# Performance work log

Measured on AMD Instinct MI355X. Metric: run time of the kernel, lower is better.

## Reference

```python
import jax, jax.numpy as jnp
import numpy as np

B, T, DFEAT = 2, 2048, 1024
DIM, DEPTH, H, DH = 512, 2, 8, 64
INNER = H * DH  # 512
MLP = 512
RED1, RED2 = DIM // 16, DIM // 32  # 32, 16
EPS = 1e-5


def _ln(x, g, b):
    m = jnp.mean(x, axis=-1, keepdims=True)
    v = jnp.mean((x - m) ** 2, axis=-1, keepdims=True)
    return (x - m) * jax.lax.rsqrt(v + EPS) * g + b


def _bn_eval(x, g, b, rm, rv):
    # x: [B, C, T]; eval-mode BatchNorm1d with running stats
    return (x - rm[:, None]) * jax.lax.rsqrt(rv[:, None] + EPS) * g[:, None] + b[:, None]


def setup_inputs() -> dict:
    key = jax.random.key(0)
    ks = iter(jax.random.split(key, 64))
    rn = lambda shape, s=0.02: (jax.random.normal(next(ks), shape, dtype=jnp.float32) * s)
    inp = {}
    inp['x'] = jax.random.normal(next(ks), (B, T, DFEAT), dtype=jnp.float32)
    # Temporal embedding conv (k=3, pad=1), OIW layout
    inp['emb_w'] = rn((DIM, DFEAT, 3))
    inp['emb_b'] = jnp.zeros((DIM,), jnp.float32)
    # Transformer: stacked per-layer params [DEPTH, ...]
    inp['ln1_g'] = jnp.ones((DEPTH, DIM), jnp.float32)
    inp['ln1_b'] = jnp.zeros((DEPTH, DIM), jnp.float32)
    inp['wqkvt'] = rn((DEPTH, DIM, 4 * INNER))
    inp['wout'] = rn((DEPTH, 2 * INNER, DIM))
    inp['bout'] = jnp.zeros((DEPTH, DIM), jnp.float32)
    inp['ln2_g'] = jnp.ones((DEPTH, DIM), jnp.float32)
    inp['ln2_b'] = jnp.zeros((DEPTH, DIM), jnp.float32)
    inp['w1'] = rn((DEPTH, DIM, MLP))
    inp['b1'] = jnp.zeros((DEPTH, MLP), jnp.float32)
    inp['w2'] = rn((DEPTH, MLP, DIM))
    inp['b2'] = jnp.zeros((DEPTH, DIM), jnp.float32)
    # NormalHead (k=1 convs -> pointwise), eval-mode BN params
    inp['h1_w'] = rn((RED1, DIM)); inp['h1_b'] = jnp.zeros((RED1,), jnp.float32)
    inp['bn1_g'] = jnp.ones((RED1,), jnp.float32); inp['bn1_b'] = jnp.zeros((RED1,), jnp.float32)
    inp['bn1_m'] = jnp.zeros((RED1,), jnp.float32); inp['bn1_v'] = jnp.ones((RED1,), jnp.float32)
    inp['h2_w'] = rn((RED2, RED1)); inp['h2_b'] = jnp.zeros((RED2,), jnp.float32)
    inp['bn2_g'] = jnp.ones((RED2,), jnp.float32); inp['bn2_b'] = jnp.zeros((RED2,), jnp.float32)
    inp['bn2_m'] = jnp.zeros((RED2,), jnp.float32); inp['bn2_v'] = jnp.ones((RED2,), jnp.float32)
    inp['h3_w'] = rn((1, RED2)); inp['h3_b'] = jnp.zeros((1,), jnp.float32)
    return inp


def _attention(x, wqkvt, wout, bout, attn2):
    b, n, d = x.shape
    qkvt = x @ wqkvt  # [b, n, 4*INNER]
    q, k, v, t = jnp.split(qkvt, 4, axis=-1)
    sp = lambda z: z.reshape(b, n, H, DH).transpose(0, 2, 1, 3)  # b h n d
    q, k, v, t = sp(q), sp(k), sp(v), sp(t)
    scale = DH ** -0.5
    dots = jnp.einsum('bhid,bhjd->bhij', q, k) * scale
    attn1 = jax.nn.softmax(dots, axis=-1)
    out1 = jnp.einsum('bhij,bhjd->bhid', attn1, v)
    out2 = jnp.einsum('ij,bhjd->bhid', attn2, t)
    out = jnp.concatenate([out1, out2], axis=-1)  # b h n 2*DH
    out = out.transpose(0, 2, 1, 3).reshape(b, n, 2 * INNER)
    return out @ wout + bout


def _forward(x, emb_w, emb_b, ln1_g, ln1_b, wqkvt, wout, bout, ln2_g, ln2_b,
             w1, b1, w2, b2, h1_w, h1_b, bn1_g, bn1_b, bn1_m, bn1_v,
             h2_w, h2_b, bn2_g, bn2_b, bn2_m, bn2_v, h3_w, h3_b):
    # Temporal embedding: Conv1d(k=3,pad=1) + ReLU over time axis
    xc = x.transpose(0, 2, 1)  # [B, DFEAT, T]
    emb = jax.lax.conv_general_dilated(xc, emb_w, (1,), 'SAME',
                                       dimension_numbers=('NCH', 'OIH', 'NCH'))
    emb = jax.nn.relu(emb + emb_b[None, :, None])
    h = emb.transpose(0, 2, 1)  # [B, T, DIM]
    # fixed temporal-decay attention matrix (batch/head independent)
    idx = jnp.arange(T, dtype=jnp.float32)
    tg = jnp.abs(idx[None, :] - idx[:, None])
    a2 = jnp.exp(-tg / jnp.float32(np.e))
    attn2 = a2 / a2.sum(-1)  # torch broadcast: divide along last axis
    for l in range(DEPTH):
        h = h + _attention(_ln(h, ln1_g[l], ln1_b[l]), wqkvt[l], wout[l], bout[l], attn2)
        z = _ln(h, ln2_g[l], ln2_b[l])
        z = jax.nn.gelu(z @ w1[l] + b1[l], approximate=False) @ w2[l] + b2[l]
        h = h + z
    # NormalHead on [B, DIM, T] with k=1 convs
    y = h.transpose(0, 2, 1)
    f1 = jnp.einsum('oc,bct->bot', h1_w, y) + h1_b[None, :, None]
    f2 = jnp.einsum('oc,bct->bot', h2_w, jax.nn.relu(_bn_eval(f1, bn1_g, bn1_b, bn1_m, bn1_v))) + h2_b[None, :, None]
    f3 = jnp.einsum('oc,bct->bot', h3_w, jax.nn.relu(_bn_eval(f2, bn2_g, bn2_b, bn2_m, bn2_v))) + h3_b[None, :, None]
    scores = jax.nn.sigmoid(f3)[:, 0, :]  # [B, T]
    return scores


def reference(x, emb_w, emb_b, ln1_g, ln1_b, wqkvt, wout, bout, ln2_g, ln2_b,
              w1, b1, w2, b2, h1_w, h1_b, bn1_g, bn1_b, bn1_m, bn1_v,
              h2_w, h2_b, bn2_g, bn2_b, bn2_m, bn2_v, h3_w, h3_b):
    return _forward(x, emb_w, emb_b, ln1_g, ln1_b, wqkvt, wout, bout, ln2_g, ln2_b,
                    w1, b1, w2, b2, h1_w, h1_b, bn1_g, bn1_b, bn1_m, bn1_v,
                    h2_w, h2_b, bn2_g, bn2_b, bn2_m, bn2_v, h3_w, h3_b)
```

## Files before the change

### kernel.cpp

```cpp
#include <hip/hip_runtime.h>
#include <hip/hip_bf16.h>
#include <math.h>

#define TN 2048
#define BN 2
#define DF 1024
#define DM 512
#define NHD 8
#define DHD 64
#define INV_E 0.36787944117144233f
#define R_DECAY 0.69220062755534635f

typedef float f32x4 __attribute__((ext_vector_type(4)));
typedef __bf16 bf16x8 __attribute__((ext_vector_type(8)));
typedef unsigned short ushort8 __attribute__((ext_vector_type(8)));
typedef unsigned short ushort4v __attribute__((ext_vector_type(4)));
typedef unsigned int u32x4 __attribute__((ext_vector_type(4)));
typedef unsigned short u16;
typedef unsigned int u32;

__device__ inline u16 f2bf(float f) {
    __hip_bfloat16 b = __float2bfloat16(f);
    return __builtin_bit_cast(u16, b);
}
__device__ inline float bf2f(u16 u) {
    unsigned int x = ((unsigned int)u) << 16;
    return __builtin_bit_cast(float, x);
}
__device__ inline bf16x8 ldbf8(const u16* p) {
    return __builtin_bit_cast(bf16x8, *(const ushort8*)p);
}

struct WtrAll {
    const float* src[8];
    u16* dst[8];
    int K[8], N[8], start[8], mask[8], shift[8];
};

__global__ __launch_bounds__(256) void wtr_all_kernel(WtrAll a) {
    __shared__ u16 tile[64][67];
    int bid = blockIdx.x;
    int w = 0;
#pragma unroll
    for (int i = 1; i < 8; ++i)
        if (bid >= a.start[i]) w = i;
    const float* src = a.src[w];
    u16* dst = a.dst[w];
    int K = a.K[w], N = a.N[w];
    int t0 = bid - a.start[w];
    int bx = t0 & a.mask[w], by = t0 >> a.shift[w];
    int t = threadIdx.x;
    int tr = t >> 4, tc = (t & 15) * 4;
#pragma unroll
    for (int rr = 0; rr < 4; ++rr) {
        int kl = tr + rr * 16;
        float4 v = *(const float4*)&src[(size_t)(by * 64 + kl) * N + bx * 64 + tc];
        tile[kl][tc + 0] = f2bf(v.x);
        tile[kl][tc + 1] = f2bf(v.y);
        tile[kl][tc + 2] = f2bf(v.z);
        tile[kl][tc + 3] = f2bf(v.w);
    }
    __syncthreads();
#pragma unroll
    for (int rr = 0; rr < 4; ++rr) {
        int nl = tr + rr * 16;
        ushort4v o;
#pragma unroll
        for (int q = 0; q < 4; ++q) o[q] = tile[tc + q][nl];
        *(ushort4v*)&dst[(size_t)(bx * 64 + nl) * K + by * 64 + tc] = o;
    }
}

__global__ __launch_bounds__(256) void emb_tr_kernel(const float* __restrict__ w,
                                                     u16* __restrict__ dst) {
    int idx = blockIdx.x * 256 + threadIdx.x;
    if (idx >= DM * 3 * DF) return;
    int o = idx / (3 * DF);
    int rem = idx - o * 3 * DF;
    int tap = rem / DF, i = rem - tap * DF;
    dst[idx] = f2bf(w[(size_t)o * 3 * DF + i * 3 + tap]);
}

__global__ __launch_bounds__(256) void sinv_kernel(float* __restrict__ sinv) {
    int j = blockIdx.x * 256 + threadIdx.x;
    if (j >= TN) return;
    float r = __expf(-INV_E);
    float inv1mr = 1.f / (1.f - r);
    float a = (1.f - __expf(-(float)(j + 1) * INV_E)) * inv1mr;
    float b = (r - __expf(-(float)(TN - j) * INV_E)) * inv1mr;
    sinv[j] = 1.f / (a + b);
}

__global__ __launch_bounds__(256) void xshift_kernel(const float* __restrict__ x,
                                                     u16* __restrict__ xs) {
    int idx = blockIdx.x * 256 + threadIdx.x;
    if (idx >= BN * TN * 3 * DF / 8) return;
    int row = idx / (3 * DF / 8);
    int kc = (idx - row * (3 * DF / 8)) * 8;
    int b = row >> 11, t = row & (TN - 1);
    int tap = kc / DF, i = kc - tap * DF;
    int tt = t + tap - 1;
    ushort8 o;
    if (tt < 0 || tt >= TN) {
        for (int q = 0; q < 8; ++q) o[q] = 0;
    } else {
        const float4* p = (const float4*)&x[((size_t)b * TN + tt) * DF + i];
        float4 v0 = p[0], v1 = p[1];
        o[0] = f2bf(v0.x); o[1] = f2bf(v0.y); o[2] = f2bf(v0.z); o[3] = f2bf(v0.w);
        o[4] = f2bf(v1.x); o[5] = f2bf(v1.y); o[6] = f2bf(v1.z); o[7] = f2bf(v1.w);
    }
    *(ushort8*)&xs[(size_t)row * 3 * DF + kc] = o;
}

template <int MODE, int BM, int BNT>
__global__ __launch_bounds__(256) void gemm2(const u16* __restrict__ A,
                                             const u16* __restrict__ Bt,
                                             const float* __restrict__ bias,
                                             const float* resid, void* outp,
                                             int M, int N, int K) {
    constexpr int MR = BM / 32, NR = BNT / 32;
    constexpr int PA = BM / 64, PB = BNT / 64;
    __shared__ __align__(16) u16 As[2][BM][72];
    __shared__ __align__(16) u16 Bs[2][BNT][72];
    int tid = threadIdx.x;
    int lane = tid & 63, wid = tid >> 6;
    int m0 = blockIdx.y * BM, n0 = blockIdx.x * BNT;
    int wm = (wid >> 1) * (BM / 2), wn = (wid & 1) * (BNT / 2);
    int fr = lane & 15, kq = (lane >> 4) * 8;
    int srow = tid >> 2, scol = (tid & 3) * 16;
    f32x4 acc[MR][NR] = {};
    const u16* Ap = A + (size_t)(m0 + srow) * K + scol;
    const u16* Bp = Bt + (size_t)(n0 + srow) * K + scol;
    ushort8 ra[PA][2], rb[PB][2];
#pragma unroll
    for (int p = 0; p < PA; ++p) {
        ra[p][0] = *(const ushort8*)(Ap + (size_t)p * 64 * K);
        ra[p][1] = *(const ushort8*)(Ap + (size_t)p * 64 * K + 8);
    }
#pragma unroll
    for (int p = 0; p < PB; ++p) {
        rb[p][0] = *(const ushort8*)(Bp + (size_t)p * 64 * K);
        rb[p][1] = *(const ushort8*)(Bp + (size_t)p * 64 * K + 8);
    }
    int nt = K >> 6;
    int pb = 0;
    for (int t = 0; t < nt; ++t) {
#pragma unroll
        for (int p = 0; p < PA; ++p) {
            *(ushort8*)&As[pb][srow + p * 64][scol] = ra[p][0];
            *(ushort8*)&As[pb][srow + p * 64][scol + 8] = ra[p][1];
        }
#pragma unroll
        for (int p = 0; p < PB; ++p) {
            *(ushort8*)&Bs[pb][srow + p * 64][scol] = rb[p][0];
            *(ushort8*)&Bs[pb][srow + p * 64][scol + 8] = rb[p][1];
        }
        __syncthreads();
        if (t + 1 < nt) {
            int ko = (t + 1) << 6;
#pragma unroll
            for (int p = 0; p < PA; ++p) {
                ra[p][0] = *(const ushort8*)(Ap + (size_t)p * 64 * K + ko);
                ra[p][1] = *(const ushort8*)(Ap + (size_t)p * 64 * K + ko + 8);
            }
#pragma unroll
            for (int p = 0; p < PB; ++p) {
                rb[p][0] = *(const ushort8*)(Bp + (size_t)p * 64 * K + ko);
                rb[p][1] = *(const ushort8*)(Bp + (size_t)p * 64 * K + ko + 8);
            }
        }
#pragma unroll
        for (int kc = 0; kc < 2; ++kc) {
            bf16x8 af[MR], bf[NR];
#pragma unroll
            for (int a = 0; a < MR; ++a) af[a] = ldbf8(&As[pb][wm + a * 16 + fr][kc * 32 + kq]);
#pragma unroll
            for (int b = 0; b < NR; ++b) bf[b] = ldbf8(&Bs[pb][wn + b * 16 + fr][kc * 32 + kq]);
#pragma unroll
            for (int a = 0; a < MR; ++a)
#pragma unroll
                for (int b = 0; b < NR; ++b)
                    acc[a][b] = __builtin_amdgcn_mfma_f32_16x16x32_bf16(af[a], bf[b], acc[a][b], 0, 0, 0);
        }
        pb ^= 1;
    }
    int rq = (lane >> 4) * 4;
#pragma unroll
    for (int a = 0; a < MR; ++a)
#pragma unroll
        for (int b = 0; b < NR; ++b) {
            int col = n0 + wn + b * 16 + fr;
            float bv = (MODE & 1) ? bias[col] : 0.f;
#pragma unroll
            for (int r = 0; r < 4; ++r) {
                int row = m0 + wm + a * 16 + rq + r;
                float v = acc[a][b][r] + bv;
                if (MODE & 2) v = fmaxf(v, 0.f);
                if (MODE & 4) v = 0.5f * v * (1.f + erff(v * 0.7071067811865476f));
                if (MODE & 8) v += resid[(size_t)row * N + col];
                if (MODE & 16) ((float*)outp)[(size_t)row * N + col] = v;
                else           ((u16*)outp)[(size_t)row * N + col] = f2bf(v);
            }
        }
}

__global__ __launch_bounds__(256) void ln_kernel(const float* __restrict__ h,
                                                 const float* __restrict__ g,
                                                 const float* __restrict__ bta,
                                                 u16* __restrict__ outp) {
    int lane = threadIdx.x & 63, wid = threadIdx.x >> 6;
    int row = blockIdx.x * 4 + wid;
    const float4* xp = (const float4*)(h + (size_t)row * DM + lane * 8);
    float4 v0 = xp[0], v1 = xp[1];
    float v[8] = {v0.x, v0.y, v0.z, v0.w, v1.x, v1.y, v1.z, v1.w};
    float s = 0.f;
#pragma unroll
    for (int i = 0; i < 8; ++i) s += v[i];
    for (int sft = 1; sft < 64; sft <<= 1) s += __shfl_xor(s, sft, 64);
    float mean = s * (1.f / DM);
    float q = 0.f;
#pragma unroll
    for (int i = 0; i < 8; ++i) { float d = v[i] - mean; q += d * d; }
    for (int sft = 1; sft < 64; sft <<= 1) q += __shfl_xor(q, sft, 64);
    float rs = rsqrtf(q * (1.f / DM) + 1e-5f);
    ushort8 o;
#pragma unroll
    for (int i = 0; i < 8; ++i) {
        float y = (v[i] - mean) * rs * g[lane * 8 + i] + bta[lane * 8 + i];
        o[i] = f2bf(y);
    }
    *(ushort8*)&outp[(size_t)row * DM + lane * 8] = o;
}

__global__ __launch_bounds__(256, 6) void attn_split(const u16* __restrict__ qkvt,
                                                     u16* __restrict__ po,
                                                     float* __restrict__ pl) {
    __shared__ __align__(16) u16 Ks[64][72];
    __shared__ __align__(16) u16 Vs[64][72];
    int tid = threadIdx.x;
    int lane = tid & 63, wid = tid >> 6;
    int bid = blockIdx.x;
    int cc = bid & 3, qb = (bid >> 2) & 31, hh = (bid >> 7) & 7, b = bid >> 10;
    int fr = lane & 15, kq = (lane >> 4) * 8, rq = (lane >> 4) * 4;

    int qrow = qb * 64 + wid * 16 + fr;
    bf16x8 aq[2];
#pragma unroll
    for (int kc = 0; kc < 2; ++kc) {
        bf16x8 t = ldbf8(&qkvt[((size_t)(b * TN + qrow)) * 2048 + hh * 64 + kc * 32 + kq]);
        bf16x8 sc;
#pragma unroll
        for (int i = 0; i < 8; ++i) sc[i] = (__bf16)(0.125f * (float)t[i]);
        aq[kc] = sc;
    }

    f32x4 o[4];
#pragma unroll
    for (int cb = 0; cb < 4; ++cb) o[cb] = f32x4{0.f, 0.f, 0.f, 0.f};
    float rsum = 0.f;

    int srow = tid >> 3, scol = (tid & 7) * 8;
    int vxw = ((scol >> 3) & 7) << 3;
    int i01 = (fr + ((lane & 16) << 1)) << 2;
    int i23 = i01 + 64;
    bool hi2 = (lane & 32) != 0;

    const u16* kvbase = qkvt + ((size_t)(b * TN + cc * 512 + srow)) * 2048 + hh * 64 + scol;

    ushort8 rk[2], rv[2];
    rk[0] = *(const ushort8*)(kvbase + 512);
    rk[1] = *(const ushort8*)(kvbase + 512 + (size_t)32 * 2048);
    rv[0] = *(const ushort8*)(kvbase + 1024);
    rv[1] = *(const ushort8*)(kvbase + 1024 + (size_t)32 * 2048);

    for (int t = 0; t < 8; ++t) {
        __syncthreads();
#pragma unroll
        for (int half = 0; half < 2; ++half) {
            int jr = srow + half * 32;
            *(ushort8*)&Ks[jr][scol] = rk[half];
            int jc = jr ^ vxw;
#pragma unroll
            for (int i = 0; i < 8; ++i) Vs[scol + i][jc] = rv[half][i];
        }
        __syncthreads();
        if (t < 7) {
            const u16* kb2 = kvbase + (size_t)(t + 1) * 64 * 2048;
            rk[0] = *(const ushort8*)(kb2 + 512);
            rk[1] = *(const ushort8*)(kb2 + 512 + (size_t)32 * 2048);
            rv[0] = *(const ushort8*)(kb2 + 1024);
            rv[1] = *(const ushort8*)(kb2 + 1024 + (size_t)32 * 2048);
        }
        u32 pkr[4][2];
#pragma unroll
        for (int jb = 0; jb < 4; ++jb) {
            f32x4 sa = f32x4{0.f, 0.f, 0.f, 0.f};
#pragma unroll
            for (int kc = 0; kc < 2; ++kc) {
                bf16x8 bk = ldbf8(&Ks[jb * 16 + fr][kc * 32 + kq]);
                sa = __builtin_amdgcn_mfma_f32_16x16x32_bf16(bk, aq[kc], sa, 0, 0, 0);
            }
            float p0 = __expf(sa[0]), p1 = __expf(sa[1]);
            float p2 = __expf(sa[2]), p3 = __expf(sa[3]);
            rsum += (p0 + p1) + (p2 + p3);
            pkr[jb][0] = ((u32)f2bf(p1) << 16) | (u32)f2bf(p0);
            pkr[jb][1] = ((u32)f2bf(p3) << 16) | (u32)f2bf(p2);
        }
        bf16x8 pa[2];
#pragma unroll
        for (int kc = 0; kc < 2; ++kc) {
            u32 a0 = (u32)__builtin_amdgcn_ds_bpermute(i01, (int)pkr[kc * 2][0]);
            u32 b0 = (u32)__builtin_amdgcn_ds_bpermute(i01, (int)pkr[kc * 2 + 1][0]);
            u32 a1 = (u32)__builtin_amdgcn_ds_bpermute(i01, (int)pkr[kc * 2][1]);
            u32 b1 = (u32)__builtin_amdgcn_ds_bpermute(i01, (int)pkr[kc * 2 + 1][1]);
            u32 a2 = (u32)__builtin_amdgcn_ds_bpermute(i23, (int)pkr[kc * 2][0]);
            u32 b2 = (u32)__builtin_amdgcn_ds_bpermute(i23, (int)pkr[kc * 2 + 1][0]);
            u32 a3 = (u32)__builtin_amdgcn_ds_bpermute(i23, (int)pkr[kc * 2][1]);
            u32 b3 = (u32)__builtin_amdgcn_ds_bpermute(i23, (int)pkr[kc * 2 + 1][1]);
            u32x4 w;
            w[0] = hi2 ? b0 : a0;
            w[1] = hi2 ? b1 : a1;
            w[2] = hi2 ? b2 : a2;
            w[3] = hi2 ? b3 : a3;
            pa[kc] = __builtin_bit_cast(bf16x8, w);
        }
#pragma unroll
        for (int cb = 0; cb < 4; ++cb)
#pragma unroll
            for (int kc = 0; kc < 2; ++kc) {
                int vrow = cb * 16 + fr;
                bf16x8 bv = ldbf8(&Vs[vrow][(kc * 32 + kq) ^ (((vrow >> 3) & 7) << 3)]);
                o[cb] = __builtin_amdgcn_mfma_f32_16x16x32_bf16(pa[kc], bv, o[cb], 0, 0, 0);
            }
    }
    rsum += __shfl_xor(rsum, 16, 64);
    rsum += __shfl_xor(rsum, 32, 64);
#pragma unroll
    for (int r = 0; r < 4; ++r) {
        int grow = (b * NHD + hh) * TN + qb * 64 + wid * 16 + rq + r;
        size_t pidx = (size_t)grow * 4 + cc;
#pragma unroll
        for (int cb = 0; cb < 4; ++cb)
            po[pidx * 64 + cb * 16 + fr] = f2bf(o[cb][r]);
    }
    if (lane < 16) {
        int grow = (b * NHD + hh) * TN + qb * 64 + wid * 16 + fr;
        pl[(size_t)grow * 4 + cc] = rsum;
    }
}

#define BCH 32
__global__ __launch_bounds__(256) void postattn_kernel(const u16* __restrict__ po,
                                                       const float* __restrict__ pl,
                                                       const u16* __restrict__ qkvt,
                                                       const float* __restrict__ sinv,
                                                       u16* __restrict__ attcat) {
    int bid = blockIdx.x;
    if (bid < BN * NHD * TN / 4) {
        int lane = threadIdx.x & 63, wid = threadIdx.x >> 6;
        int R = bid * 4 + wid;
        float l = 0.f, ov = 0.f;
#pragma unroll
        for (int cc = 0; cc < 4; ++cc) {
            l += pl[R * 4 + cc];
            ov += bf2f(po[((size_t)R * 4 + cc) * 64 + lane]);
        }
        int bh = R >> 11, q = R & (TN - 1);
        int b = bh >> 3, hh = bh & 7;
        attcat[((size_t)(b * TN + q)) * 1024 + hh * 128 + lane] = f2bf(ov / l);
    } else {
        int t2 = (bid - BN * NHD * TN / 4) * 256 + threadIdx.x;
        int c = t2 & 511;
        int rest = t2 >> 9;
        int chunk = rest & 63;
        int b = rest >> 6;
        int i0 = chunk * BCH;
        const float r = R_DECAY;
        const u16* tcol = qkvt + 1536 + c;
        float regs[BCH];
        float st = 0.f;
        for (int j = i0 - 32; j < i0; ++j) {
            if (j >= 0) st = r * st + sinv[j] * bf2f(tcol[(size_t)(b * TN + j) * 2048]);
        }
#pragma unroll
        for (int k = 0; k < BCH; ++k) {
            int j = i0 + k;
            st = r * st + sinv[j] * bf2f(tcol[(size_t)(b * TN + j) * 2048]);
            regs[k] = st;
        }
        st = 0.f;
        for (int j = i0 + BCH + 31; j >= i0 + BCH; --j) {
            if (j < TN) st = r * st + sinv[j] * bf2f(tcol[(size_t)(b * TN + j) * 2048]);
        }
#pragma unroll
        for (int k = BCH - 1; k >= 0; --k) {
            int j = i0 + k;
            regs[k] += r * st;
            st = r * st + sinv[j] * bf2f(tcol[(size_t)(b * TN + j) * 2048]);
        }
        int outcol = (c >> 6) * 128 + 64 + (c & 63);
#pragma unroll
        for (int k = 0; k < BCH; ++k)
            attcat[((size_t)(b * TN + i0 + k)) * 1024 + outcol] = f2bf(regs[k]);
    }
}

__global__ __launch_bounds__(256) void head_kernel(
    const float* __restrict__ h, const float* __restrict__ h1w, const float* __restrict__ h1b,
    const float* __restrict__ bn1g, const float* __restrict__ bn1b,
    const float* __restrict__ bn1m, const float* __restrict__ bn1v,
    const float* __restrict__ h2w, const float* __restrict__ h2b,
    const float* __restrict__ bn2g, const float* __restrict__ bn2b,
    const float* __restrict__ bn2m, const float* __restrict__ bn2v,
    const float* __restrict__ h3w, const float* __restrict__ h3b,
    float* __restrict__ outp) {
    int lane = threadIdx.x & 63, wid = threadIdx.x >> 6;
    int idx = blockIdx.x * 4 + wid;
    const float4* xp = (const float4*)(h + (size_t)idx * DM + lane * 8);
    float4 v0 = xp[0], v1 = xp[1];
    float v[8] = {v0.x, v0.y, v0.z, v0.w, v1.x, v1.y, v1.z, v1.w};
    float a1[32];
#pragma unroll
    for (int o = 0; o < 32; ++o) {
        const float4* wp = (const float4*)(h1w + (size_t)o * DM + lane * 8);
        float4 w0 = wp[0], w1v = wp[1];
        a1[o] = w0.x * v[0] + w0.y * v[1] + w0.z * v[2] + w0.w * v[3] +
                w1v.x * v[4] + w1v.y * v[5] + w1v.z * v[6] + w1v.w * v[7];
    }
    for (int sft = 1; sft < 64; sft <<= 1) {
#pragma unroll
        for (int o = 0; o < 32; ++o) a1[o] += __shfl_xor(a1[o], sft, 64);
    }
    float r1[32];
#pragma unroll
    for (int o = 0; o < 32; ++o) {
        float f = a1[o] + h1b[o];
        f = (f - bn1m[o]) * rsqrtf(bn1v[o] + 1e-5f) * bn1g[o] + bn1b[o];
        r1[o] = fmaxf(f, 0.f);
    }
    float r2[16];
#pragma unroll
    for (int p = 0; p < 16; ++p) {
        float s = h2b[p];
#pragma unroll
        for (int o = 0; o < 32; ++o) s = fmaf(h2w[p * 32 + o], r1[o], s);
        s = (s - bn2m[p]) * rsqrtf(bn2v[p] + 1e-5f) * bn2g[p] + bn2b[p];
        r2[p] = fmaxf(s, 0.f);
    }
    float f3 = h3b[0];
#pragma unroll
    for (int p = 0; p < 16; ++p) f3 = fmaf(h3w[p], r2[p], f3);
    if (lane == 0) outp[idx] = 1.f / (1.f + __expf(-f3));
}

extern "C" void kernel_launch(void* const* d_in, const int* in_sizes, int n_in,
                              void* d_out, int out_size, void* d_ws, size_t ws_size,
                              hipStream_t stream) {
    const float* x     = (const float*)d_in[0];
    const float* emb_w = (const float*)d_in[1];
    const float* emb_b = (const float*)d_in[2];
    const float* ln1_g = (const float*)d_in[3];
    const float* ln1_b = (const float*)d_in[4];
    const float* wqkvt = (const float*)d_in[5];
    const float* wout  = (const float*)d_in[6];
    const float* bout  = (const float*)d_in[7];
    const float* ln2_g = (const float*)d_in[8];
    const float* ln2_b = (const float*)d_in[9];
    const float* w1    = (const float*)d_in[10];
    const float* b1    = (const float*)d_in[11];
    const float* w2    = (const float*)d_in[12];
    const float* b2    = (const float*)d_in[13];
    const float* h1w   = (const float*)d_in[14];
    const float* h1b   = (const float*)d_in[15];
    const float* bn1g  = (const float*)d_in[16];
    const float* bn1b  = (const float*)d_in[17];
    const float* bn1m  = (const float*)d_in[18];
    const float* bn1v  = (const float*)d_in[19];
    const float* h2w   = (const float*)d_in[20];
    const float* h2b   = (const float*)d_in[21];
    const float* bn2g  = (const float*)d_in[22];
    const float* bn2b  = (const float*)d_in[23];
    const float* bn2m  = (const float*)d_in[24];
    const float* bn2v  = (const float*)d_in[25];
    const float* h3w   = (const float*)d_in[26];
    const float* h3b   = (const float*)d_in[27];
    float* outp = (float*)d_out;

    char* ws = (char*)d_ws;
    size_t off = 0;
    auto take = [&](size_t bytes) {
        char* p = ws + off;
        off = (off + bytes + 255) & ~(size_t)255;
        return p;
    };
    const size_t MB = 1024 * 1024;
    float* h    = (float*)take((size_t)BN * TN * DM * 4);
    char* Pr    = take(18 * MB);
    u16* attcat = (u16*)take((size_t)BN * TN * 1024 * 2);
    float* sinv = (float*)take(TN * 4);
    u16* embwt  = (u16*)take((size_t)DM * 3 * DF * 2);
    u16* wqt    = (u16*)take((size_t)2 * 2048 * DM * 2);
    u16* woutt  = (u16*)take((size_t)2 * DM * 1024 * 2);
    u16* w1t    = (u16*)take((size_t)2 * DM * DM * 2);
    u16* w2t    = (u16*)take((size_t)2 * DM * DM * 2);
    u16* U      = (u16*)take((size_t)BN * TN * 3 * DF * 2);
    u16* xs = U;
    u16* qkvtb = U;
    u16* xln  = (u16*)Pr;
    u16* z1   = (u16*)(Pr + 4 * MB);
    float* pl = (float*)Pr;
    u16* po   = (u16*)(Pr + 1 * MB);
    (void)ws_size; (void)in_sizes; (void)n_in; (void)out_size;

    emb_tr_kernel<<<dim3(DM * 3 * DF / 256), dim3(256), 0, stream>>>(emb_w, embwt);
    {
        WtrAll a;
        int cur = 0;
        for (int l = 0; l < 2; ++l) {
            int e = l * 4;
            a.src[e + 0] = wqkvt + (size_t)l * 512 * 2048; a.dst[e + 0] = wqt + (size_t)l * 2048 * 512;
            a.K[e + 0] = 512;  a.N[e + 0] = 2048; a.start[e + 0] = cur; a.mask[e + 0] = 31; a.shift[e + 0] = 5; cur += 256;
            a.src[e + 1] = wout + (size_t)l * 1024 * 512;  a.dst[e + 1] = woutt + (size_t)l * 512 * 1024;
            a.K[e + 1] = 1024; a.N[e + 1] = 512;  a.start[e + 1] = cur; a.mask[e + 1] = 7;  a.shift[e + 1] = 3; cur += 128;
            a.src[e + 2] = w1 + (size_t)l * 512 * 512;     a.dst[e + 2] = w1t + (size_t)l * 512 * 512;
            a.K[e + 2] = 512;  a.N[e + 2] = 512;  a.start[e + 2] = cur; a.mask[e + 2] = 7;  a.shift[e + 2] = 3; cur += 64;
            a.src[e + 3] = w2 + (size_t)l * 512 * 512;     a.dst[e + 3] = w2t + (size_t)l * 512 * 512;
            a.K[e + 3] = 512;  a.N[e + 3] = 512;  a.start[e + 3] = cur; a.mask[e + 3] = 7;  a.shift[e + 3] = 3; cur += 64;
        }
        wtr_all_kernel<<<dim3(cur), dim3(256), 0, stream>>>(a);
    }
    sinv_kernel<<<dim3(TN / 256), dim3(256), 0, stream>>>(sinv);
    xshift_kernel<<<dim3(BN * TN * 3 * DF / 8 / 256), dim3(256), 0, stream>>>(x, xs);

    gemm2<19, 64, 64><<<dim3(DM / 64, BN * TN / 64), dim3(256), 0, stream>>>(
        xs, embwt, emb_b, nullptr, h, BN * TN, DM, 3 * DF);

    for (int l = 0; l < 2; ++l) {
        ln_kernel<<<dim3(BN * TN / 4), dim3(256), 0, stream>>>(h, ln1_g + l * DM, ln1_b + l * DM, xln);
        gemm2<0, 128, 128><<<dim3(2048 / 128, BN * TN / 128), dim3(256), 0, stream>>>(
            xln, wqt + (size_t)l * 2048 * 512, nullptr, nullptr, qkvtb, BN * TN, 2048, DM);
        attn_split<<<dim3(BN * NHD * (TN / 64) * 4), dim3(256), 0, stream>>>(qkvtb, po, pl);
        postattn_kernel<<<dim3(BN * NHD * TN / 4 + BN * 512 * (TN / BCH) / 256), dim3(256), 0, stream>>>(
            po, pl, qkvtb, sinv, attcat);
        gemm2<25, 64, 64><<<dim3(DM / 64, BN * TN / 64), dim3(256), 0, stream>>>(
            attcat, woutt + (size_t)l * 512 * 1024, bout + l * DM, h, h, BN * TN, DM, 1024);
        ln_kernel<<<dim3(BN * TN / 4), dim3(256), 0, stream>>>(h, ln2_g + l * DM, ln2_b + l * DM, xln);
        gemm2<5, 64, 64><<<dim3(DM / 64, BN * TN / 64), dim3(256), 0, stream>>>(
            xln, w1t + (size_t)l * 512 * 512, b1 + l * DM, nullptr, z1, BN * TN, DM, DM);
        gemm2<25, 64, 64><<<dim3(DM / 64, BN * TN / 64), dim3(256), 0, stream>>>(
            z1, w2t + (size_t)l * 512 * 512, b2 + l * DM, h, h, BN * TN, DM, DM);
    }
    head_kernel<<<dim3(BN * TN / 4), dim3(256), 0, stream>>>(
        h, h1w, h1b, bn1g, bn1b, bn1m, bn1v, h2w, h2b, bn2g, bn2b, bn2m, bn2v, h3w, h3b, outp);
}
```

Baseline: 347.9 us.

## Load GEMM tiles directly to LDS with XOR swizzle, enlarge M tiles

Replaces the register-staged, double-buffered GEMM tile loading with global_load_lds, which writes directly into shared memory. An XOR swizzle on the 16-byte chunks avoids bank conflicts without padding. Most 64x64 GEMM launches move to 128x64 tiles. The aim is lower register pressure and fewer LDS write instructions, but the single buffer exposes load latency with two barriers per k-step, and the larger tiles halve the block count.

```diff
diff --git a/kernel.cpp b/kernel.cpp
--- a/kernel.cpp
+++ b/kernel.cpp
@@ -29,6 +29,11 @@
 }
 __device__ inline bf16x8 ldbf8(const u16* p) {
     return __builtin_bit_cast(bf16x8, *(const ushort8*)p);
+}
+__device__ inline void gl_lds16(const u16* g, u16* l) {
+    __builtin_amdgcn_global_load_lds(
+        (const __attribute__((address_space(1))) unsigned int*)g,
+        (__attribute__((address_space(3))) unsigned int*)l, 16, 0, 0);
 }
 
 struct WtrAll {
@@ -113,76 +118,59 @@
 }
 
 template <int MODE, int BM, int BNT>
-__global__ __launch_bounds__(256) void gemm2(const u16* __restrict__ A,
+__global__ __launch_bounds__(256) void gemm3(const u16* __restrict__ A,
                                              const u16* __restrict__ Bt,
                                              const float* __restrict__ bias,
                                              const float* resid, void* outp,
                                              int M, int N, int K) {
     constexpr int MR = BM / 32, NR = BNT / 32;
-    constexpr int PA = BM / 64, PB = BNT / 64;
-    __shared__ __align__(16) u16 As[2][BM][72];
-    __shared__ __align__(16) u16 Bs[2][BNT][72];
+    __shared__ __align__(16) u16 As[BM][64];
+    __shared__ __align__(16) u16 Bs[BNT][64];
     int tid = threadIdx.x;
     int lane = tid & 63, wid = tid >> 6;
     int m0 = blockIdx.y * BM, n0 = blockIdx.x * BNT;
     int wm = (wid >> 1) * (BM / 2), wn = (wid & 1) * (BNT / 2);
-    int fr = lane & 15, kq = (lane >> 4) * 8;
-    int srow = tid >> 2, scol = (tid & 3) * 16;
+    int fr = lane & 15, g = lane >> 4;
+    int lrow8 = lane >> 3, slot = lane & 7;
     f32x4 acc[MR][NR] = {};
-    const u16* Ap = A + (size_t)(m0 + srow) * K + scol;
-    const u16* Bp = Bt + (size_t)(n0 + srow) * K + scol;
-    ushort8 ra[PA][2], rb[PB][2];
-#pragma unroll
-    for (int p = 0; p < PA; ++p) {
-        ra[p][0] = *(const ushort8*)(Ap + (size_t)p * 64 * K);
-        ra[p][1] = *(const ushort8*)(Ap + (size_t)p * 64 * K + 8);
-    }
-#pragma unroll
-    for (int p = 0; p < PB; ++p) {
-        rb[p][0] = *(const ushort8*)(Bp + (size_t)p * 64 * K);
-        rb[p][1] = *(const ushort8*)(Bp + (size_t)p * 64 * K + 8);
-    }
     int nt = K >> 6;
-    int pb = 0;
     for (int t = 0; t < nt; ++t) {
-#pragma unroll
-        for (int p = 0; p < PA; ++p) {
-            *(ushort8*)&As[pb][srow + p * 64][scol] = ra[p][0];
-            *(ushort8*)&As[pb][srow + p * 64][scol + 8] = ra[p][1];
-        }
-#pragma unroll
-        for (int p = 0; p < PB; ++p) {
-            *(ushort8*)&Bs[pb][srow + p * 64][scol] = rb[p][0];
-            *(ushort8*)&Bs[pb][srow + p * 64][scol + 8] = rb[p][1];
-        }
+        int k0 = t << 6;
         __syncthreads();
-        if (t + 1 < nt) {
-            int ko = (t + 1) << 6;
-#pragma unroll
-            for (int p = 0; p < PA; ++p) {
-                ra[p][0] = *(const ushort8*)(Ap + (size_t)p * 64 * K + ko);
-                ra[p][1] = *(const ushort8*)(Ap + (size_t)p * 64 * K + ko + 8);
-            }
-#pragma unroll
-            for (int p = 0; p < PB; ++p) {
-                rb[p][0] = *(const ushort8*)(Bp + (size_t)p * 64 * K + ko);
-                rb[p][1] = *(const ushort8*)(Bp + (size_t)p * 64 * K + ko + 8);
-            }
-        }
+#pragma unroll
+        for (int ii = 0; ii < BM / 32; ++ii) {
+            int R0 = wid * (BM / 4) + ii * 8;
+            int r = R0 + lrow8;
+            const u16* gsrc = A + (size_t)(m0 + r) * K + k0 + ((slot ^ (r & 7)) * 8);
+            gl_lds16(gsrc, &As[R0][0]);
+        }
+#pragma unroll
+        for (int ii = 0; ii < BNT / 32; ++ii) {
+            int R0 = wid * (BNT / 4) + ii * 8;
+            int r = R0 + lrow8;
+            const u16* gsrc = Bt + (size_t)(n0 + r) * K + k0 + ((slot ^ (r & 7)) * 8);
+            gl_lds16(gsrc, &Bs[R0][0]);
+        }
+        __syncthreads();
 #pragma unroll
         for (int kc = 0; kc < 2; ++kc) {
             bf16x8 af[MR], bf[NR];
 #pragma unroll
-            for (int a = 0; a < MR; ++a) af[a] = ldbf8(&As[pb][wm + a * 16 + fr][kc * 32 + kq]);
-#pragma unroll
-            for (int b = 0; b < NR; ++b) bf[b] = ldbf8(&Bs[pb][wn + b * 16 + fr][kc * 32 + kq]);
+            for (int a = 0; a < MR; ++a) {
+                int R = wm + a * 16 + fr;
+                af[a] = ldbf8(&As[R][((kc * 4 + g) ^ (fr & 7)) * 8]);
+            }
+#pragma unroll
+            for (int b = 0; b < NR; ++b) {
+                int R = wn + b * 16 + fr;
+                bf[b] = ldbf8(&Bs[R][((kc * 4 + g) ^ (fr & 7)) * 8]);
+            }
 #pragma unroll
             for (int a = 0; a < MR; ++a)
 #pragma unroll
                 for (int b = 0; b < NR; ++b)
                     acc[a][b] = __builtin_amdgcn_mfma_f32_16x16x32_bf16(af[a], bf[b], acc[a][b], 0, 0, 0);
         }
-        pb ^= 1;
     }
     int rq = (lane >> 4) * 4;
 #pragma unroll
@@ -532,22 +520,22 @@
     sinv_kernel<<<dim3(TN / 256), dim3(256), 0, stream>>>(sinv);
     xshift_kernel<<<dim3(BN * TN * 3 * DF / 8 / 256), dim3(256), 0, stream>>>(x, xs);
 
-    gemm2<19, 64, 64><<<dim3(DM / 64, BN * TN / 64), dim3(256), 0, stream>>>(
+    gemm3<19, 128, 64><<<dim3(DM / 64, BN * TN / 128), dim3(256), 0, stream>>>(
         xs, embwt, emb_b, nullptr, h, BN * TN, DM, 3 * DF);
 
     for (int l = 0; l < 2; ++l) {
         ln_kernel<<<dim3(BN * TN / 4), dim3(256), 0, stream>>>(h, ln1_g + l * DM, ln1_b + l * DM, xln);
-        gemm2<0, 128, 128><<<dim3(2048 / 128, BN * TN / 128), dim3(256), 0, stream>>>(
+        gemm3<0, 128, 128><<<dim3(2048 / 128, BN * TN / 128), dim3(256), 0, stream>>>(
             xln, wqt + (size_t)l * 2048 * 512, nullptr, nullptr, qkvtb, BN * TN, 2048, DM);
         attn_split<<<dim3(BN * NHD * (TN / 64) * 4), dim3(256), 0, stream>>>(qkvtb, po, pl);
         postattn_kernel<<<dim3(BN * NHD * TN / 4 + BN * 512 * (TN / BCH) / 256), dim3(256), 0, stream>>>(
             po, pl, qkvtb, sinv, attcat);
-        gemm2<25, 64, 64><<<dim3(DM / 64, BN * TN / 64), dim3(256), 0, stream>>>(
+        gemm3<25, 128, 64><<<dim3(DM / 64, BN * TN / 128), dim3(256), 0, stream>>>(
             attcat, woutt + (size_t)l * 512 * 1024, bout + l * DM, h, h, BN * TN, DM, 1024);
         ln_kernel<<<dim3(BN * TN / 4), dim3(256), 0, stream>>>(h, ln2_g + l * DM, ln2_b + l * DM, xln);
-        gemm2<5, 64, 64><<<dim3(DM / 64, BN * TN / 64), dim3(256), 0, stream>>>(
+        gemm3<5, 128, 64><<<dim3(DM / 64, BN * TN / 128), dim3(256), 0, stream>>>(
             xln, w1t + (size_t)l * 512 * 512, b1 + l * DM, nullptr, z1, BN * TN, DM, DM);
-        gemm2<25, 64, 64><<<dim3(DM / 64, BN * TN / 64), dim3(256), 0, stream>>>(
+        gemm3<25, 128, 64><<<dim3(DM / 64, BN * TN / 128), dim3(256), 0, stream>>>(
             z1, w2t + (size_t)l * 512 * 512, b2 + l * DM, h, h, BN * TN, DM, DM);
     }
     head_kernel<<<dim3(BN * TN / 4), dim3(256), 0, stream>>>(
```

Result: slower. 399.3 us (+14.8%).

## Double query rows per attention block and swizzle GEMM blocks across XCDs

Applied to the files above, without the earlier changes.

Each attention block now handles 128 query rows instead of 64, with every wave computing two 16-row query sub-tiles against each shared K/V tile. This halves the K/V global loads and LDS staging per query row, at the cost of more registers (launch bounds lowered from 6 to 4 blocks per CU) and half as many blocks. Separately, the GEMM launches move to a 1D grid with a remap that gives each group of 8 blocks (blockIdx mod 8) a contiguous tile range. The apparent goal is better L2 locality on the multi-XCD MI355X, assuming blocks are dealt round-robin across the 8 XCDs.

```diff
diff --git a/kernel.cpp b/kernel.cpp
--- a/kernel.cpp
+++ b/kernel.cpp
@@ -112,7 +112,7 @@
     *(ushort8*)&xs[(size_t)row * 3 * DF + kc] = o;
 }
 
-template <int MODE, int BM, int BNT>
+template <int MODE, int BM, int BNT, int LOG_NX>
 __global__ __launch_bounds__(256) void gemm2(const u16* __restrict__ A,
                                              const u16* __restrict__ Bt,
                                              const float* __restrict__ bias,
@@ -124,7 +124,10 @@
     __shared__ __align__(16) u16 Bs[2][BNT][72];
     int tid = threadIdx.x;
     int lane = tid & 63, wid = tid >> 6;
-    int m0 = blockIdx.y * BM, n0 = blockIdx.x * BNT;
+    int cpx = gridDim.x >> 3;
+    int swz = (blockIdx.x & 7) * cpx + (blockIdx.x >> 3);
+    int n0 = (swz & ((1 << LOG_NX) - 1)) * BNT;
+    int m0 = (swz >> LOG_NX) * BM;
     int wm = (wid >> 1) * (BM / 2), wn = (wid & 1) * (BNT / 2);
     int fr = lane & 15, kq = (lane >> 4) * 8;
     int srow = tid >> 2, scol = (tid & 3) * 16;
@@ -232,7 +235,7 @@
     *(ushort8*)&outp[(size_t)row * DM + lane * 8] = o;
 }
 
-__global__ __launch_bounds__(256, 6) void attn_split(const u16* __restrict__ qkvt,
+__global__ __launch_bounds__(256, 4) void attn_split(const u16* __restrict__ qkvt,
                                                      u16* __restrict__ po,
                                                      float* __restrict__ pl) {
     __shared__ __align__(16) u16 Ks[64][72];
@@ -240,24 +243,24 @@
     int tid = threadIdx.x;
     int lane = tid & 63, wid = tid >> 6;
     int bid = blockIdx.x;
-    int cc = bid & 3, qb = (bid >> 2) & 31, hh = (bid >> 7) & 7, b = bid >> 10;
+    int cc = bid & 3, qb = (bid >> 2) & 15, hh = (bid >> 6) & 7, b = bid >> 9;
     int fr = lane & 15, kq = (lane >> 4) * 8, rq = (lane >> 4) * 4;
 
-    int qrow = qb * 64 + wid * 16 + fr;
-    bf16x8 aq[2];
-#pragma unroll
-    for (int kc = 0; kc < 2; ++kc) {
-        bf16x8 t = ldbf8(&qkvt[((size_t)(b * TN + qrow)) * 2048 + hh * 64 + kc * 32 + kq]);
-        bf16x8 sc;
-#pragma unroll
-        for (int i = 0; i < 8; ++i) sc[i] = (__bf16)(0.125f * (float)t[i]);
-        aq[kc] = sc;
-    }
-
-    f32x4 o[4];
-#pragma unroll
-    for (int cb = 0; cb < 4; ++cb) o[cb] = f32x4{0.f, 0.f, 0.f, 0.f};
-    float rsum = 0.f;
+    bf16x8 aq[2][2];
+#pragma unroll
+    for (int s = 0; s < 2; ++s)
+#pragma unroll
+        for (int kc = 0; kc < 2; ++kc) {
+            int qrow = qb * 128 + wid * 32 + s * 16 + fr;
+            bf16x8 t = ldbf8(&qkvt[((size_t)(b * TN + qrow)) * 2048 + hh * 64 + kc * 32 + kq]);
+            bf16x8 sc;
+#pragma unroll
+            for (int i = 0; i < 8; ++i) sc[i] = (__bf16)(0.125f * (float)t[i]);
+            aq[s][kc] = sc;
+        }
+
+    f32x4 o[2][4] = {};
+    float rsum[2] = {0.f, 0.f};
 
     int srow = tid >> 3, scol = (tid & 7) * 8;
     int vxw = ((scol >> 3) & 7) << 3;
@@ -291,61 +294,83 @@
             rv[0] = *(const ushort8*)(kb2 + 1024);
             rv[1] = *(const ushort8*)(kb2 + 1024 + (size_t)32 * 2048);
         }
-        u32 pkr[4][2];
+        u32 pkr[2][4][2];
 #pragma unroll
         for (int jb = 0; jb < 4; ++jb) {
-            f32x4 sa = f32x4{0.f, 0.f, 0.f, 0.f};
+            f32x4 sa0 = f32x4{0.f, 0.f, 0.f, 0.f};
+            f32x4 sa1 = f32x4{0.f, 0.f, 0.f, 0.f};
 #pragma unroll
             for (int kc = 0; kc < 2; ++kc) {
                 bf16x8 bk = ldbf8(&Ks[jb * 16 + fr][kc * 32 + kq]);
-                sa = __builtin_amdgcn_mfma_f32_16x16x32_bf16(bk, aq[kc], sa, 0, 0, 0);
-            }
-            float p0 = __expf(sa[0]), p1 = __expf(sa[1]);
-            float p2 = __expf(sa[2]), p3 = __expf(sa[3]);
-            rsum += (p0 + p1) + (p2 + p3);
-            pkr[jb][0] = ((u32)f2bf(p1) << 16) | (u32)f2bf(p0);
-            pkr[jb][1] = ((u32)f2bf(p3) << 16) | (u32)f2bf(p2);
-        }
-        bf16x8 pa[2];
-#pragma unroll
-        for (int kc = 0; kc < 2; ++kc) {
-            u32 a0 = (u32)__builtin_amdgcn_ds_bpermute(i01, (int)pkr[kc * 2][0]);
-            u32 b0 = (u32)__builtin_amdgcn_ds_bpermute(i01, (int)pkr[kc * 2 + 1][0]);
-            u32 a1 = (u32)__builtin_amdgcn_ds_bpermute(i01, (int)pkr[kc * 2][1]);
-            u32 b1 = (u32)__builtin_amdgcn_ds_bpermute(i01, (int)pkr[kc * 2 + 1][1]);
-            u32 a2 = (u32)__builtin_amdgcn_ds_bpermute(i23, (int)pkr[kc * 2][0]);
-            u32 b2 = (u32)__builtin_amdgcn_ds_bpermute(i23, (int)pkr[kc * 2 + 1][0]);
-            u32 a3 = (u32)__builtin_amdgcn_ds_bpermute(i23, (int)pkr[kc * 2][1]);
-            u32 b3 = (u32)__builtin_amdgcn_ds_bpermute(i23, (int)pkr[kc * 2 + 1][1]);
-            u32x4 w;
-            w[0] = hi2 ? b0 : a0;
-            w[1] = hi2 ? b1 : a1;
-            w[2] = hi2 ? b2 : a2;
-            w[3] = hi2 ? b3 : a3;
-            pa[kc] = __builtin_bit_cast(bf16x8, w);
-        }
+                sa0 = __builtin_amdgcn_mfma_f32_16x16x32_bf16(bk, aq[0][kc], sa0, 0, 0, 0);
+                sa1 = __builtin_amdgcn_mfma_f32_16x16x32_bf16(bk, aq[1][kc], sa1, 0, 0, 0);
+            }
+            {
+                float p0 = __expf(sa0[0]), p1 = __expf(sa0[1]);
+                float p2 = __expf(sa0[2]), p3 = __expf(sa0[3]);
+                rsum[0] += (p0 + p1) + (p2 + p3);
+                pkr[0][jb][0] = ((u32)f2bf(p1) << 16) | (u32)f2bf(p0);
+                pkr[0][jb][1] = ((u32)f2bf(p3) << 16) | (u32)f2bf(p2);
+            }
+            {
+                float p0 = __expf(sa1[0]), p1 = __expf(sa1[1]);
+                float p2 = __expf(sa1[2]), p3 = __expf(sa1[3]);
+                rsum[1] += (p0 + p1) + (p2 + p3);
+                pkr[1][jb][0] = ((u32)f2bf(p1) << 16) | (u32)f2bf(p0);
+                pkr[1][jb][1] = ((u32)f2bf(p3) << 16) | (u32)f2bf(p2);
+            }
+        }
+        bf16x8 pa[2][2];
+#pragma unroll
+        for (int s = 0; s < 2; ++s)
+#pragma unroll
+            for (int kc = 0; kc < 2; ++kc) {
+                u32 a0 = (u32)__builtin_amdgcn_ds_bpermute(i01, (int)pkr[s][kc * 2][0]);
+                u32 b0 = (u32)__builtin_amdgcn_ds_bpermute(i01, (int)pkr[s][kc * 2 + 1][0]);
+                u32 a1 = (u32)__builtin_amdgcn_ds_bpermute(i01, (int)pkr[s][kc * 2][1]);
+                u32 b1 = (u32)__builtin_amdgcn_ds_bpermute(i01, (int)pkr[s][kc * 2 + 1][1]);
+                u32 a2 = (u32)__builtin_amdgcn_ds_bpermute(i23, (int)pkr[s][kc * 2][0]);
+                u32 b2 = (u32)__builtin_amdgcn_ds_bpermute(i23, (int)pkr[s][kc * 2 + 1][0]);
+                u32 a3 = (u32)__builtin_amdgcn_ds_bpermute(i23, (int)pkr[s][kc * 2][1]);
+                u32 b3 = (u32)__builtin_amdgcn_ds_bpermute(i23, (int)pkr[s][kc * 2 + 1][1]);
+                u32x4 w;
+                w[0] = hi2 ? b0 : a0;
+                w[1] = hi2 ? b1 : a1;
+                w[2] = hi2 ? b2 : a2;
+                w[3] = hi2 ? b3 : a3;
+                pa[s][kc] = __builtin_bit_cast(bf16x8, w);
+            }
 #pragma unroll
         for (int cb = 0; cb < 4; ++cb)
 #pragma unroll
             for (int kc = 0; kc < 2; ++kc) {
                 int vrow = cb * 16 + fr;
                 bf16x8 bv = ldbf8(&Vs[vrow][(kc * 32 + kq) ^ (((vrow >> 3) & 7) << 3)]);
-                o[cb] = __builtin_amdgcn_mfma_f32_16x16x32_bf16(pa[kc], bv, o[cb], 0, 0, 0);
-            }
-    }
-    rsum += __shfl_xor(rsum, 16, 64);
-    rsum += __shfl_xor(rsum, 32, 64);
-#pragma unroll
-    for (int r = 0; r < 4; ++r) {
-        int grow = (b * NHD + hh) * TN + qb * 64 + wid * 16 + rq + r;
-        size_t pidx = (size_t)grow * 4 + cc;
-#pragma unroll
-        for (int cb = 0; cb < 4; ++cb)
-            po[pidx * 64 + cb * 16 + fr] = f2bf(o[cb][r]);
-    }
+                o[0][cb] = __builtin_amdgcn_mfma_f32_16x16x32_bf16(pa[0][kc], bv, o[0][cb], 0, 0, 0);
+                o[1][cb] = __builtin_amdgcn_mfma_f32_16x16x32_bf16(pa[1][kc], bv, o[1][cb], 0, 0, 0);
+            }
+    }
+#pragma unroll
+    for (int s = 0; s < 2; ++s) {
+        rsum[s] += __shfl_xor(rsum[s], 16, 64);
+        rsum[s] += __shfl_xor(rsum[s], 32, 64);
+    }
+#pragma unroll
+    for (int s = 0; s < 2; ++s)
+#pragma unroll
+        for (int r = 0; r < 4; ++r) {
+            int grow = (b * NHD + hh) * TN + qb * 128 + wid * 32 + s * 16 + rq + r;
+            size_t pidx = (size_t)grow * 4 + cc;
+#pragma unroll
+            for (int cb = 0; cb < 4; ++cb)
+                po[pidx * 64 + cb * 16 + fr] = f2bf(o[s][cb][r]);
+        }
     if (lane < 16) {
-        int grow = (b * NHD + hh) * TN + qb * 64 + wid * 16 + fr;
-        pl[(size_t)grow * 4 + cc] = rsum;
+#pragma unroll
+        for (int s = 0; s < 2; ++s) {
+            int grow = (b * NHD + hh) * TN + qb * 128 + wid * 32 + s * 16 + fr;
+            pl[(size_t)grow * 4 + cc] = rsum[s];
+        }
     }
 }
 
@@ -532,22 +557,22 @@
     sinv_kernel<<<dim3(TN / 256), dim3(256), 0, stream>>>(sinv);
     xshift_kernel<<<dim3(BN * TN * 3 * DF / 8 / 256), dim3(256), 0, stream>>>(x, xs);
 
-    gemm2<19, 64, 64><<<dim3(DM / 64, BN * TN / 64), dim3(256), 0, stream>>>(
+    gemm2<19, 64, 64, 3><<<dim3((DM / 64) * (BN * TN / 64)), dim3(256), 0, stream>>>(
         xs, embwt, emb_b, nullptr, h, BN * TN, DM, 3 * DF);
 
     for (int l = 0; l < 2; ++l) {
         ln_kernel<<<dim3(BN * TN / 4), dim3(256), 0, stream>>>(h, ln1_g + l * DM, ln1_b + l * DM, xln);
-        gemm2<0, 128, 128><<<dim3(2048 / 128, BN * TN / 128), dim3(256), 0, stream>>>(
+        gemm2<0, 128, 128, 4><<<dim3((2048 / 128) * (BN * TN / 128)), dim3(256), 0, stream>>>(
             xln, wqt + (size_t)l * 2048 * 512, nullptr, nullptr, qkvtb, BN * TN, 2048, DM);
-        attn_split<<<dim3(BN * NHD * (TN / 64) * 4), dim3(256), 0, stream>>>(qkvtb, po, pl);
+        attn_split<<<dim3(BN * NHD * (TN / 128) * 4), dim3(256), 0, stream>>>(qkvtb, po, pl);
         postattn_kernel<<<dim3(BN * NHD * TN / 4 + BN * 512 * (TN / BCH) / 256), dim3(256), 0, stream>>>(
             po, pl, qkvtb, sinv, attcat);
-        gemm2<25, 64, 64><<<dim3(DM / 64, BN * TN / 64), dim3(256), 0, stream>>>(
+        gemm2<25, 64, 64, 3><<<dim3((DM / 64) * (BN * TN / 64)), dim3(256), 0, stream>>>(
             attcat, woutt + (size_t)l * 512 * 1024, bout + l * DM, h, h, BN * TN, DM, 1024);
         ln_kernel<<<dim3(BN * TN / 4), dim3(256), 0, stream>>>(h, ln2_g + l * DM, ln2_b + l * DM, xln);
-        gemm2<5, 64, 64><<<dim3(DM / 64, BN * TN / 64), dim3(256), 0, stream>>>(
+        gemm2<5, 64, 64, 3><<<dim3((DM / 64) * (BN * TN / 64)), dim3(256), 0, stream>>>(
             xln, w1t + (size_t)l * 512 * 512, b1 + l * DM, nullptr, z1, BN * TN, DM, DM);
-        gemm2<25, 64, 64><<<dim3(DM / 64, BN * TN / 64), dim3(256), 0, stream>>>(
+        gemm2<25, 64, 64, 3><<<dim3((DM / 64) * (BN * TN / 64)), dim3(256), 0, stream>>>(
             z1, w2t + (size_t)l * 512 * 512, b2 + l * DM, h, h, BN * TN, DM, DM);
     }
     head_kernel<<<dim3(BN * TN / 4), dim3(256), 0, stream>>>(
```

Result: faster. 330.5 us (-5.0%).
